# Kernel tuning notes

Measured on AMD Instinct MI355X. Metric: run time of the kernel, lower is better.

## Reference

```python
import jax, jax.numpy as jnp
import numpy as np

B, S, H, NH, HD, V = 2, 2048, 1024, 16, 64, 32000
BASE = 10000.0
NEG = jnp.finfo(jnp.float32).min


def setup_inputs() -> dict:
    key = jax.random.key(0)
    ks = jax.random.split(key, 12)
    batch = jax.random.randint(ks[0], (B, S), 0, V)
    positions = jnp.broadcast_to(jnp.arange(S), (B, S))
    lengths = jax.random.randint(ks[1], (B,), 1, S + 1)  # >=1 to avoid fully-masked rows
    sc = 1.0 / np.sqrt(H)
    emb = jax.random.normal(ks[2], (V, H), dtype=jnp.float32) * 0.02
    wq = jax.random.normal(ks[3], (H, NH * HD), dtype=jnp.float32) * sc
    bq = jnp.zeros((NH * HD,), jnp.float32)
    wk = jax.random.normal(ks[4], (H, NH * HD), dtype=jnp.float32) * sc
    bk = jnp.zeros((NH * HD,), jnp.float32)
    wv = jax.random.normal(ks[5], (H, NH * HD), dtype=jnp.float32) * sc
    bv = jnp.zeros((NH * HD,), jnp.float32)
    wo = jax.random.normal(ks[6], (NH * HD, H), dtype=jnp.float32) * sc
    bo = jnp.zeros((H,), jnp.float32)
    return dict(batch=batch, positions=positions, lengths=lengths, emb=emb,
                wq=wq, bq=bq, wk=wk, bk=bk, wv=wv, bv=bv, wo=wo, bo=bo)


def _rope(x, positions):
    # x: [B, NH, S, HD]; positions: [B, S] int
    inv_freq = 1.0 / (BASE ** (jnp.arange(0, HD, 2, dtype=jnp.float32) / HD))  # [HD/2]
    freqs = positions.astype(jnp.float32)[..., None] * inv_freq               # [B, S, HD/2]
    ang = jnp.concatenate([freqs, freqs], axis=-1)                            # [B, S, HD]
    cos = jnp.cos(ang)[:, None]                                               # [B, 1, S, HD]
    sin = jnp.sin(ang)[:, None]
    x1, x2 = x[..., :HD // 2], x[..., HD // 2:]
    rot = jnp.concatenate([-x2, x1], axis=-1)
    return x * cos + rot * sin


def reference(batch, positions, lengths, emb, wq, bq, wk, bk, wv, bv, wo, bo):
    h = emb[batch]                                                 # [B, S, H]
    q = (h @ wq + bq).reshape(B, S, NH, HD).transpose(0, 2, 1, 3)  # [B, NH, S, HD]
    k = (h @ wk + bk).reshape(B, S, NH, HD).transpose(0, 2, 1, 3)
    v = (h @ wv + bv).reshape(B, S, NH, HD).transpose(0, 2, 1, 3)
    q = _rope(q, positions)
    k = _rope(k, positions)
    scores = jnp.einsum('bhqd,bhkd->bhqk', q, k) / np.sqrt(HD)     # [B, NH, S, S]
    causal = jnp.triu(jnp.full((S, S), NEG, jnp.float32), 1)
    pad = jnp.where(jnp.arange(S)[None, :] < lengths[:, None], 0.0, NEG)  # [B, S]
    mask = pad[:, None, None, :] + causal[None, None]              # [B, 1, S, S]
    attn = jax.nn.softmax(scores + mask, axis=-1)
    out = jnp.einsum('bhqk,bhkd->bhqd', attn, v)                   # [B, NH, S, HD]
    out = out.transpose(0, 2, 1, 3).reshape(B, S, NH * HD)
    return out @ wo + bo                                           # [B, S, H]
```

## Files before the change

### kernel.cpp

```cpp
#include <hip/hip_runtime.h>
#include <hip/hip_bf16.h>
#include <cstdint>

#define DEVINL __device__ __forceinline__

typedef __attribute__((ext_vector_type(8))) short short8;
typedef __attribute__((ext_vector_type(4))) float f32x4;

constexpr int B_ = 2, S_ = 2048, H_ = 1024, NH_ = 16, HD_ = 64;
constexpr int M_ = B_ * S_;
constexpr float SC2 = 0.18033688f;

DEVINL float bf2f(unsigned short h) {
    unsigned u = ((unsigned)h) << 16;
    float f; __builtin_memcpy(&f, &u, 4); return f;
}
DEVINL unsigned short f2bf(float f) {
    unsigned u; __builtin_memcpy(&u, &f, 4);
    u += 0x7FFFu + ((u >> 16) & 1u);
    return (unsigned short)(u >> 16);
}
DEVINL unsigned pk2bf(float a, float b) {
    __hip_bfloat162 h = __float22bfloat162_rn(float2{a, b});
    unsigned u; __builtin_memcpy(&u, &h, 4); return u;
}
DEVINL float fexp2(float x) {
#if __has_builtin(__builtin_amdgcn_exp2f)
    return __builtin_amdgcn_exp2f(x);
#else
    return exp2f(x);
#endif
}
DEVINL float ldin(const void* p, size_t i, int fp32) {
    return fp32 ? ((const float*)p)[i] : bf2f(((const unsigned short*)p)[i]);
}
DEVINL void gl16(const void* g, void* l) {
    __builtin_amdgcn_global_load_lds(
        (const __attribute__((address_space(1))) unsigned int*)g,
        (__attribute__((address_space(3))) unsigned int*)l, 16, 0, 0);
}
DEVINL f32x4 mfma16(short8 a, short8 b, f32x4 c) {
    return __builtin_amdgcn_mfma_f32_16x16x32_bf16(a, b, c, 0, 0, 0);
}
DEVINL void fsincos(float rev01, float* sn, float* cs) {
#if __has_builtin(__builtin_amdgcn_sinf) && __has_builtin(__builtin_amdgcn_cosf)
    *sn = __builtin_amdgcn_sinf(rev01);
    *cs = __builtin_amdgcn_cosf(rev01);
#else
    float a = rev01 * 6.28318530717958647692f;
    *sn = __sinf(a); *cs = __cosf(a);
#endif
}
DEVINL int detect_fp32(const unsigned short* emb, int t) {
    unsigned short hw = emb[2 * t];
    unsigned e = (hw >> 7) & 0xFFu;
    int s = (((e >= 90u) && (e <= 126u)) || ((hw & 0x7FFFu) == 0u)) ? 1 : 0;
    #pragma unroll
    for (int o = 1; o < 64; o <<= 1) s += __shfl_xor(s, o);
    __shared__ int cnt[4];
    if ((t & 63) == 0) cnt[t >> 6] = s;
    __syncthreads();
    return ((cnt[0] + cnt[1] + cnt[2] + cnt[3]) > 192) ? 0 : 1;
}

__global__ __launch_bounds__(256) void k_transw(const void* w0, const void* w1,
                                                const void* w2, const void* w3,
                                                const void* bq, const void* bk,
                                                const void* bv, const void* bo,
                                                const unsigned short* __restrict__ emb,
                                                int* __restrict__ flag,
                                                float* __restrict__ biasws,
                                                unsigned short* __restrict__ wT) {
    __shared__ float tile[32][33];
    int tx = threadIdx.x, ty = threadIdx.y, t = ty * 32 + tx;
    int fp32 = detect_fp32(emb, t);
    int mat = blockIdx.z;
    if (mat == 0 && blockIdx.y == 0) {
        if (blockIdx.x == 0 && t == 0) flag[0] = fp32;
        if (blockIdx.x < 16) {
            int i = blockIdx.x * 256 + t;
            const void* src = (i < 1024) ? bq : (i < 2048) ? bk : (i < 3072) ? bv : bo;
            biasws[i] = ldin(src, (size_t)(i & 1023), fp32);
        }
    }
    const void* w = (mat == 0) ? w0 : (mat == 1) ? w1 : (mat == 2) ? w2 : w3;
    int n0 = blockIdx.x * 32, k0 = blockIdx.y * 32;
    for (int i = ty; i < 32; i += 8)
        tile[i][tx] = ldin(w, (size_t)(k0 + i) * 1024 + n0 + tx, fp32);
    __syncthreads();
    unsigned short* dst = wT + (size_t)mat * 1024 * 1024;
    for (int i = ty; i < 32; i += 8)
        dst[(size_t)(n0 + i) * 1024 + k0 + tx] = f2bf(tile[tx][i]);
}

__global__ __launch_bounds__(256) void k_gather(const int* __restrict__ batch,
                                                const void* __restrict__ emb,
                                                const int* __restrict__ flag,
                                                unsigned short* __restrict__ h) {
    if (flag[0] == 0) return;
    int row = blockIdx.x, t = threadIdx.x;
    int tok = batch[row];
    const float4* s = (const float4*)((const float*)emb + (size_t)tok * H_);
    float4 x = s[t];
    unsigned long long pk = (unsigned long long)f2bf(x.x)
                          | ((unsigned long long)f2bf(x.y) << 16)
                          | ((unsigned long long)f2bf(x.z) << 32)
                          | ((unsigned long long)f2bf(x.w) << 48);
    ((unsigned long long*)(h + (size_t)row * H_))[t] = pk;
}

__global__ __launch_bounds__(256) void k_gemm_qkv(const unsigned short* __restrict__ embb,
                                                  const unsigned short* __restrict__ hbuf,
                                                  const int* __restrict__ batch,
                                                  const unsigned short* __restrict__ Bt,
                                                  const float* __restrict__ bias,
                                                  const int* __restrict__ positions,
                                                  const int* __restrict__ flag,
                                                  unsigned short* __restrict__ qo,
                                                  unsigned short* __restrict__ ko,
                                                  unsigned short* __restrict__ vt) {
    constexpr int K = 1024;
    __shared__ alignas(16) unsigned short As[2][128 * 32];
    __shared__ alignas(16) unsigned short Bs[2][128 * 32];
    int t = threadIdx.x, lane = t & 63, quad = lane >> 4, n16 = lane & 15;
    int w = t >> 6, wm = w >> 1, wn = w & 1;
    int m0 = blockIdx.y * 128, n0 = blockIdx.x * 128;
    int fp32 = flag[0];
    int r0 = t >> 2, r1 = 64 + r0;
    int ka = (t & 3) * 8;
    const unsigned short* a0;
    const unsigned short* a1;
    if (fp32) {
        a0 = hbuf + (size_t)(m0 + r0) * K;
        a1 = hbuf + (size_t)(m0 + r1) * K;
    } else {
        a0 = embb + (size_t)batch[m0 + r0] * K;
        a1 = embb + (size_t)batch[m0 + r1] * K;
    }
    const unsigned short* b0 = Bt + (size_t)(n0 + r0) * K;
    const unsigned short* b1 = Bt + (size_t)(n0 + r1) * K;
    f32x4 acc[4][4];
    #pragma unroll
    for (int mi = 0; mi < 4; mi++)
        #pragma unroll
        for (int ni = 0; ni < 4; ni++) acc[mi][ni] = (f32x4){0.f, 0.f, 0.f, 0.f};
    for (int k0 = 0; k0 < K; k0 += 64) {
        __syncthreads();
        gl16(a0 + k0 + ka,      &As[0][t * 8]);
        gl16(a1 + k0 + ka,      &As[0][(t + 256) * 8]);
        gl16(a0 + k0 + 32 + ka, &As[1][t * 8]);
        gl16(a1 + k0 + 32 + ka, &As[1][(t + 256) * 8]);
        gl16(b0 + k0 + ka,      &Bs[0][t * 8]);
        gl16(b1 + k0 + ka,      &Bs[0][(t + 256) * 8]);
        gl16(b0 + k0 + 32 + ka, &Bs[1][t * 8]);
        gl16(b1 + k0 + 32 + ka, &Bs[1][(t + 256) * 8]);
        __syncthreads();
        #pragma unroll
        for (int ks = 0; ks < 2; ks++) {
            short8 af[4], bfr[4];
            #pragma unroll
            for (int mi = 0; mi < 4; mi++)
                af[mi] = *(const short8*)&As[ks][(wm * 64 + mi * 16 + n16) * 32 + quad * 8];
            #pragma unroll
            for (int ni = 0; ni < 4; ni++)
                bfr[ni] = *(const short8*)&Bs[ks][(wn * 64 + ni * 16 + n16) * 32 + quad * 8];
            #pragma unroll
            for (int mi = 0; mi < 4; mi++)
                #pragma unroll
                for (int ni = 0; ni < 4; ni++)
                    acc[mi][ni] = mfma16(af[mi], bfr[ni], acc[mi][ni]);
        }
    }
    int colbase = n0 + wn * 64;
    int buf = colbase >> 10;
    int cc = colbase & 1023;
    float bb[4];
    #pragma unroll
    for (int ni = 0; ni < 4; ni++) bb[ni] = bias[colbase + ni * 16 + n16];
    if (buf == 2) {
        #pragma unroll
        for (int mi = 0; mi < 4; mi++) {
            int row = m0 + wm * 64 + mi * 16 + quad * 4;
            int bb_ = row >> 11;
            int s0 = row & 2047;
            int pos = (s0 & ~31) + quad * 8 + (mi & 1) * 4;
            #pragma unroll
            for (int ni = 0; ni < 4; ni++) {
                int f = cc + ni * 16 + n16;
                unsigned long long pk =
                      (unsigned long long)pk2bf(acc[mi][ni][0] + bb[ni], acc[mi][ni][1] + bb[ni])
                    | ((unsigned long long)pk2bf(acc[mi][ni][2] + bb[ni], acc[mi][ni][3] + bb[ni]) << 32);
                *(unsigned long long*)(vt + ((size_t)(bb_ * 1024 + f)) * 2048 + pos) = pk;
            }
        }
    } else {
        unsigned short* out = (buf == 0) ? qo : ko;
        float osc = (buf == 0) ? SC2 : 1.0f;
        float revf[2];
        #pragma unroll
        for (int ni = 0; ni < 2; ni++) {
            float d = (float)(ni * 16 + n16);
            revf[ni] = __expf(d * -0.28782313f) * 0.15915494f;
        }
        #pragma unroll
        for (int mi = 0; mi < 4; mi++) {
            int row0 = m0 + wm * 64 + mi * 16 + quad * 4;
            #pragma unroll
            for (int i = 0; i < 4; i++) {
                int row = row0 + i;
                float pos = (float)positions[row];
                #pragma unroll
                for (int ni = 0; ni < 2; ni++) {
                    float rev = pos * revf[ni];
                    float fr = rev - floorf(rev);
                    float sn, cs; fsincos(fr, &sn, &cs);
                    float x1 = (acc[mi][ni][i] + bb[ni]) * osc;
                    float x2 = (acc[mi][ni + 2][i] + bb[ni + 2]) * osc;
                    out[(size_t)row * 1024 + cc + ni * 16 + n16] = f2bf(x1 * cs - x2 * sn);
                    out[(size_t)row * 1024 + cc + (ni + 2) * 16 + n16] = f2bf(x2 * cs + x1 * sn);
                }
            }
        }
    }
}

__global__ __launch_bounds__(256) void k_attn(const unsigned short* __restrict__ q,
                                              const unsigned short* __restrict__ k_,
                                              const unsigned short* __restrict__ vt,
                                              const int* __restrict__ lengths,
                                              unsigned short* __restrict__ o) {
    __shared__ alignas(16) unsigned short Ks[2][64 * 64];
    __shared__ alignas(16) unsigned short Vs[2][64 * 64];
    int bx = blockIdx.x;
    int j = bx & 15, hh = (bx >> 4) & 15, b = bx >> 8;
    int t = threadIdx.x, w = t >> 6, lane = t & 63, quad = lane >> 4, n16 = lane & 15;
    int len = lengths[b];
    int tile0 = j, tile1 = 31 - j;
    int kend0 = min(tile0 * 64 + 64, len);
    int kend1 = min(tile1 * 64 + 64, len);
    int nkt = (kend1 + 63) >> 6;
    int qrow0 = tile0 * 64 + w * 16 + n16;
    int qrow1 = tile1 * 64 + w * 16 + n16;
    int limit0 = min(qrow0, len - 1);
    int limit1 = min(qrow1, len - 1);
    int tbw0 = tile0 * 64 + w * 16;
    int tbw1 = tile1 * 64 + w * 16;
    short8 qf[2][2];
    {
        size_t qa = ((size_t)(b * S_ + qrow0)) * H_ + hh * 64 + quad * 8;
        size_t qb2 = ((size_t)(b * S_ + qrow1)) * H_ + hh * 64 + quad * 8;
        qf[0][0] = *(const short8*)(q + qa);  qf[0][1] = *(const short8*)(q + qa + 32);
        qf[1][0] = *(const short8*)(q + qb2); qf[1][1] = *(const short8*)(q + qb2 + 32);
    }
    f32x4 oa[2][4];
    float l_[2] = {0.f, 0.f};
    #pragma unroll
    for (int s = 0; s < 2; s++)
        #pragma unroll
        for (int nb = 0; nb < 4; nb++) oa[s][nb] = (f32x4){0.f, 0.f, 0.f, 0.f};
    const unsigned short* kbase = k_ + ((size_t)b * S_) * H_ + hh * 64;
    const unsigned short* vbase = vt + ((size_t)(b * 1024 + hh * 64)) * 2048;
    int sr0 = t >> 3, sc0 = (t & 7) ^ (sr0 & 7);
    int sr1 = (t + 256) >> 3, sc1 = (t & 7) ^ (sr1 & 7);
    auto stage = [&](int kt) {
        int kb = kt * 64, bi = kt & 1;
        gl16(kbase + (size_t)(kb + sr0) * H_ + sc0 * 8, &Ks[bi][t * 8]);
        gl16(kbase + (size_t)(kb + sr1) * H_ + sc1 * 8, &Ks[bi][(t + 256) * 8]);
        gl16(vbase + (size_t)sr0 * 2048 + kb + sc0 * 8, &Vs[bi][t * 8]);
        gl16(vbase + (size_t)sr1 * 2048 + kb + sc1 * 8, &Vs[bi][(t + 256) * 8]);
    };
    stage(0);
    for (int kt = 0; kt < nkt; kt++) {
        int kb = kt * 64, bi = kt & 1;
        __syncthreads();
        if (kt + 1 < nkt) stage(kt + 1);
        const unsigned short* Kb = Ks[bi];
        const unsigned short* Vb = Vs[bi];
        short8 kf[4][2];
        #pragma unroll
        for (int st = 0; st < 4; st++)
            #pragma unroll
            for (int hf = 0; hf < 2; hf++) {
                int ky = st * 16 + n16;
                kf[st][hf] = *(const short8*)&Kb[ky * 64 + (((hf * 4 + quad) ^ (ky & 7)) * 8)];
            }
        short8 vf[2][4];
        #pragma unroll
        for (int p = 0; p < 2; p++)
            #pragma unroll
            for (int nb = 0; nb < 4; nb++) {
                int f = nb * 16 + n16;
                vf[p][nb] = *(const short8*)&Vb[f * 64 + (((p * 4 + quad) ^ (f & 7)) * 8)];
            }
        #pragma unroll
        for (int si = 0; si < 2; si++) {
            if (si == 0 && kb >= kend0) continue;
            int limit = si ? limit1 : limit0;
            int tbw = si ? tbw1 : tbw0;
            f32x4 sc[4];
            #pragma unroll
            for (int st = 0; st < 4; st++) {
                f32x4 z = (f32x4){0.f, 0.f, 0.f, 0.f};
                z = mfma16(kf[st][0], qf[si][0], z);
                z = mfma16(kf[st][1], qf[si][1], z);
                sc[st] = z;
            }
            float rs = 0.f;
            if (kb + 64 <= min(tbw, len)) {
                #pragma unroll
                for (int st = 0; st < 4; st++)
                    #pragma unroll
                    for (int i = 0; i < 4; i++) {
                        float p = fexp2(sc[st][i]);
                        rs += p;
                        sc[st][i] = p;
                    }
            } else {
                #pragma unroll
                for (int st = 0; st < 4; st++)
                    #pragma unroll
                    for (int i = 0; i < 4; i++) {
                        int kg = kb + st * 16 + quad * 4 + i;
                        float p = (kg <= limit) ? fexp2(sc[st][i]) : 0.f;
                        rs += p;
                        sc[st][i] = p;
                    }
            }
            rs += __shfl_xor(rs, 16);
            rs += __shfl_xor(rs, 32);
            l_[si] += rs;
            #pragma unroll
            for (int p = 0; p < 2; p++) {
                union { unsigned u[4]; short8 v8; } pp;
                pp.u[0] = pk2bf(sc[2 * p][0], sc[2 * p][1]);
                pp.u[1] = pk2bf(sc[2 * p][2], sc[2 * p][3]);
                pp.u[2] = pk2bf(sc[2 * p + 1][0], sc[2 * p + 1][1]);
                pp.u[3] = pk2bf(sc[2 * p + 1][2], sc[2 * p + 1][3]);
                #pragma unroll
                for (int nb = 0; nb < 4; nb++)
                    oa[si][nb] = mfma16(pp.v8, vf[p][nb], oa[si][nb]);
            }
        }
    }
    #pragma unroll
    for (int si = 0; si < 2; si++) {
        int tb = si ? tile1 : tile0;
        f32x4 rl;
        #pragma unroll
        for (int i = 0; i < 4; i++) rl[i] = 1.f / __shfl(l_[si], quad * 4 + i);
        #pragma unroll
        for (int nb = 0; nb < 4; nb++) {
            #pragma unroll
            for (int i = 0; i < 4; i++) {
                int row = tb * 64 + w * 16 + quad * 4 + i;
                o[((size_t)(b * S_ + row)) * H_ + hh * 64 + nb * 16 + n16] =
                    f2bf(oa[si][nb][i] * rl[i]);
            }
        }
    }
}

__global__ __launch_bounds__(256) void k_gemm64(const unsigned short* __restrict__ A,
                                                const unsigned short* __restrict__ Bt,
                                                const float* __restrict__ bias,
                                                unsigned short* __restrict__ Cb,
                                                float* __restrict__ Cf,
                                                const int* __restrict__ flag) {
    constexpr int K = 1024, N = 1024;
    __shared__ alignas(16) unsigned short As[2][64 * 32];
    __shared__ alignas(16) unsigned short Bs[2][128 * 32];
    int t = threadIdx.x, lane = t & 63, quad = lane >> 4, n16 = lane & 15;
    int w = t >> 6, wm = w & 1, wn = w >> 1;
    int m0 = blockIdx.y * 64, n0 = blockIdx.x * 128;
    int r0 = t >> 2, r1 = 64 + r0, ka = (t & 3) * 8;
    const unsigned short* a0 = A + (size_t)(m0 + r0) * K;
    const unsigned short* b0 = Bt + (size_t)(n0 + r0) * K;
    const unsigned short* b1 = Bt + (size_t)(n0 + r1) * K;
    f32x4 acc[2][4];
    #pragma unroll
    for (int mi = 0; mi < 2; mi++)
        #pragma unroll
        for (int ni = 0; ni < 4; ni++) acc[mi][ni] = (f32x4){0.f, 0.f, 0.f, 0.f};
    for (int k0 = 0; k0 < K; k0 += 64) {
        __syncthreads();
        gl16(a0 + k0 + ka,      &As[0][t * 8]);
        gl16(a0 + k0 + 32 + ka, &As[1][t * 8]);
        gl16(b0 + k0 + ka,      &Bs[0][t * 8]);
        gl16(b1 + k0 + ka,      &Bs[0][(t + 256) * 8]);
        gl16(b0 + k0 + 32 + ka, &Bs[1][t * 8]);
        gl16(b1 + k0 + 32 + ka, &Bs[1][(t + 256) * 8]);
        __syncthreads();
        #pragma unroll
        for (int ks = 0; ks < 2; ks++) {
            short8 af[2], bfr[4];
            #pragma unroll
            for (int mi = 0; mi < 2; mi++)
                af[mi] = *(const short8*)&As[ks][(wm * 32 + mi * 16 + n16) * 32 + quad * 8];
            #pragma unroll
            for (int ni = 0; ni < 4; ni++)
                bfr[ni] = *(const short8*)&Bs[ks][(wn * 64 + ni * 16 + n16) * 32 + quad * 8];
            #pragma unroll
            for (int mi = 0; mi < 2; mi++)
                #pragma unroll
                for (int ni = 0; ni < 4; ni++)
                    acc[mi][ni] = mfma16(af[mi], bfr[ni], acc[mi][ni]);
        }
    }
    int fp32out = (flag[0] == 1);
    #pragma unroll
    for (int mi = 0; mi < 2; mi++) {
        #pragma unroll
        for (int ni = 0; ni < 4; ni++) {
            int row = m0 + wm * 32 + mi * 16 + quad * 4;
            int col = n0 + wn * 64 + ni * 16 + n16;
            float bb = bias[col];
            #pragma unroll
            for (int i = 0; i < 4; i++) {
                float val = acc[mi][ni][i] + bb;
                size_t idx = (size_t)(row + i) * N + col;
                if (fp32out) Cf[idx] = val;
                else         Cb[idx] = f2bf(val);
            }
        }
    }
}

extern "C" void kernel_launch(void* const* d_in, const int* in_sizes, int n_in,
                              void* d_out, int out_size, void* d_ws, size_t ws_size,
                              hipStream_t stream) {
    (void)in_sizes; (void)n_in; (void)out_size; (void)ws_size;
    const int* batch     = (const int*)d_in[0];
    const int* positions = (const int*)d_in[1];
    const int* lengths   = (const int*)d_in[2];
    const void* emb = d_in[3];
    const void* wq = d_in[4];  const void* bq = d_in[5];
    const void* wk = d_in[6];  const void* bk = d_in[7];
    const void* wv = d_in[8];  const void* bv = d_in[9];
    const void* wo = d_in[10]; const void* bo = d_in[11];

    char* ws = (char*)d_ws;
    int*   flag   = (int*)ws;
    float* biasws = (float*)(ws + 4096);
    unsigned short* wT = (unsigned short*)(ws + 20480);
    size_t off = 20480 + (8ull << 20);
    unsigned short* hbuf = (unsigned short*)(ws + off); off += (8ull << 20);
    unsigned short* qb   = (unsigned short*)(ws + off); off += (8ull << 20);
    unsigned short* kb2  = (unsigned short*)(ws + off); off += (8ull << 20);
    unsigned short* vtb  = (unsigned short*)(ws + off); off += (8ull << 20);
    unsigned short* ao   = (unsigned short*)(ws + off); off += (8ull << 20);

    k_transw<<<dim3(32, 32, 4), dim3(32, 8), 0, stream>>>(
        wq, wk, wv, wo, bq, bk, bv, bo, (const unsigned short*)emb,
        flag, biasws, wT);
    k_gather<<<M_, 256, 0, stream>>>(batch, emb, flag, hbuf);

    k_gemm_qkv<<<dim3(3072 / 128, M_ / 128), 256, 0, stream>>>(
        (const unsigned short*)emb, hbuf, batch, wT, biasws, positions, flag,
        qb, kb2, vtb);

    k_attn<<<B_ * NH_ * 16, 256, 0, stream>>>(qb, kb2, vtb, lengths, ao);

    k_gemm64<<<dim3(1024 / 128, M_ / 64), 256, 0, stream>>>(
        ao, wT + (3ull << 20), biasws + 3072,
        (unsigned short*)d_out, (float*)d_out, flag);
}
```

Measured before the change: 303.0 us.

## Fuse gather into weight prep, load V directly, add MFMA priority and batch tile reversal

Merges the embedding gather kernel into the weight-transpose kernel as an extra grid slice, removing one launch. In attention, V fragments are now read straight from global memory instead of being staged through shared memory, which halves LDS traffic but makes V loads uncoalesced and synchronous. It also raises wave priority around MFMA blocks and reverses the tile order for odd batches to balance causal work across blocks. These changes trade LDS staging and a launch for possible global-latency stalls.

```diff
diff --git a/kernel.cpp b/kernel.cpp
--- a/kernel.cpp
+++ b/kernel.cpp
@@ -63,18 +63,39 @@
     return ((cnt[0] + cnt[1] + cnt[2] + cnt[3]) > 192) ? 0 : 1;
 }
 
-__global__ __launch_bounds__(256) void k_transw(const void* w0, const void* w1,
-                                                const void* w2, const void* w3,
-                                                const void* bq, const void* bk,
-                                                const void* bv, const void* bo,
-                                                const unsigned short* __restrict__ emb,
-                                                int* __restrict__ flag,
-                                                float* __restrict__ biasws,
-                                                unsigned short* __restrict__ wT) {
-    __shared__ float tile[32][33];
+__global__ __launch_bounds__(256) void k_prep(const void* w0, const void* w1,
+                                              const void* w2, const void* w3,
+                                              const void* bq, const void* bk,
+                                              const void* bv, const void* bo,
+                                              const unsigned short* __restrict__ emb,
+                                              const int* __restrict__ batch,
+                                              int* __restrict__ flag,
+                                              float* __restrict__ biasws,
+                                              unsigned short* __restrict__ wT,
+                                              unsigned short* __restrict__ hbuf) {
     int tx = threadIdx.x, ty = threadIdx.y, t = ty * 32 + tx;
     int fp32 = detect_fp32(emb, t);
-    int mat = blockIdx.z;
+    int z = blockIdx.z;
+    if (z == 4) {
+        if (!fp32) return;
+        int g = blockIdx.y * 32 + blockIdx.x;
+        int w = t >> 6, lane = t & 63;
+        int row = g * 4 + w;
+        int tok = batch[row];
+        const float4* s = (const float4*)((const float*)emb + (size_t)tok * H_);
+        unsigned long long* d = (unsigned long long*)(hbuf + (size_t)row * H_);
+        #pragma unroll
+        for (int c = 0; c < 4; c++) {
+            float4 x = s[lane + 64 * c];
+            d[lane + 64 * c] = (unsigned long long)f2bf(x.x)
+                             | ((unsigned long long)f2bf(x.y) << 16)
+                             | ((unsigned long long)f2bf(x.z) << 32)
+                             | ((unsigned long long)f2bf(x.w) << 48);
+        }
+        return;
+    }
+    __shared__ float tile[32][33];
+    int mat = z;
     if (mat == 0 && blockIdx.y == 0) {
         if (blockIdx.x == 0 && t == 0) flag[0] = fp32;
         if (blockIdx.x < 16) {
@@ -91,22 +112,6 @@
     unsigned short* dst = wT + (size_t)mat * 1024 * 1024;
     for (int i = ty; i < 32; i += 8)
         dst[(size_t)(n0 + i) * 1024 + k0 + tx] = f2bf(tile[tx][i]);
-}
-
-__global__ __launch_bounds__(256) void k_gather(const int* __restrict__ batch,
-                                                const void* __restrict__ emb,
-                                                const int* __restrict__ flag,
-                                                unsigned short* __restrict__ h) {
-    if (flag[0] == 0) return;
-    int row = blockIdx.x, t = threadIdx.x;
-    int tok = batch[row];
-    const float4* s = (const float4*)((const float*)emb + (size_t)tok * H_);
-    float4 x = s[t];
-    unsigned long long pk = (unsigned long long)f2bf(x.x)
-                          | ((unsigned long long)f2bf(x.y) << 16)
-                          | ((unsigned long long)f2bf(x.z) << 32)
-                          | ((unsigned long long)f2bf(x.w) << 48);
-    ((unsigned long long*)(h + (size_t)row * H_))[t] = pk;
 }
 
 __global__ __launch_bounds__(256) void k_gemm_qkv(const unsigned short* __restrict__ embb,
@@ -230,9 +235,9 @@
                                               const int* __restrict__ lengths,
                                               unsigned short* __restrict__ o) {
     __shared__ alignas(16) unsigned short Ks[2][64 * 64];
-    __shared__ alignas(16) unsigned short Vs[2][64 * 64];
     int bx = blockIdx.x;
-    int j = bx & 15, hh = (bx >> 4) & 15, b = bx >> 8;
+    int jraw = bx & 15, hh = (bx >> 4) & 15, b = bx >> 8;
+    int j = (b & 1) ? (15 - jraw) : jraw;
     int t = threadIdx.x, w = t >> 6, lane = t & 63, quad = lane >> 4, n16 = lane & 15;
     int len = lengths[b];
     int tile0 = j, tile1 = 31 - j;
@@ -266,8 +271,6 @@
         int kb = kt * 64, bi = kt & 1;
         gl16(kbase + (size_t)(kb + sr0) * H_ + sc0 * 8, &Ks[bi][t * 8]);
         gl16(kbase + (size_t)(kb + sr1) * H_ + sc1 * 8, &Ks[bi][(t + 256) * 8]);
-        gl16(vbase + (size_t)sr0 * 2048 + kb + sc0 * 8, &Vs[bi][t * 8]);
-        gl16(vbase + (size_t)sr1 * 2048 + kb + sc1 * 8, &Vs[bi][(t + 256) * 8]);
     };
     stage(0);
     for (int kt = 0; kt < nkt; kt++) {
@@ -275,7 +278,6 @@
         __syncthreads();
         if (kt + 1 < nkt) stage(kt + 1);
         const unsigned short* Kb = Ks[bi];
-        const unsigned short* Vb = Vs[bi];
         short8 kf[4][2];
         #pragma unroll
         for (int st = 0; st < 4; st++)
@@ -290,7 +292,7 @@
             #pragma unroll
             for (int nb = 0; nb < 4; nb++) {
                 int f = nb * 16 + n16;
-                vf[p][nb] = *(const short8*)&Vb[f * 64 + (((p * 4 + quad) ^ (f & 7)) * 8)];
+                vf[p][nb] = *(const short8*)(vbase + (size_t)f * 2048 + kb + (p * 4 + quad) * 8);
             }
         #pragma unroll
         for (int si = 0; si < 2; si++) {
@@ -298,6 +300,7 @@
             int limit = si ? limit1 : limit0;
             int tbw = si ? tbw1 : tbw0;
             f32x4 sc[4];
+            __builtin_amdgcn_s_setprio(1);
             #pragma unroll
             for (int st = 0; st < 4; st++) {
                 f32x4 z = (f32x4){0.f, 0.f, 0.f, 0.f};
@@ -305,6 +308,7 @@
                 z = mfma16(kf[st][1], qf[si][1], z);
                 sc[st] = z;
             }
+            __builtin_amdgcn_s_setprio(0);
             float rs = 0.f;
             if (kb + 64 <= min(tbw, len)) {
                 #pragma unroll
@@ -336,9 +340,11 @@
                 pp.u[1] = pk2bf(sc[2 * p][2], sc[2 * p][3]);
                 pp.u[2] = pk2bf(sc[2 * p + 1][0], sc[2 * p + 1][1]);
                 pp.u[3] = pk2bf(sc[2 * p + 1][2], sc[2 * p + 1][3]);
+                __builtin_amdgcn_s_setprio(1);
                 #pragma unroll
                 for (int nb = 0; nb < 4; nb++)
                     oa[si][nb] = mfma16(pp.v8, vf[p][nb], oa[si][nb]);
+                __builtin_amdgcn_s_setprio(0);
             }
         }
     }
@@ -449,10 +455,9 @@
     unsigned short* vtb  = (unsigned short*)(ws + off); off += (8ull << 20);
     unsigned short* ao   = (unsigned short*)(ws + off); off += (8ull << 20);
 
-    k_transw<<<dim3(32, 32, 4), dim3(32, 8), 0, stream>>>(
-        wq, wk, wv, wo, bq, bk, bv, bo, (const unsigned short*)emb,
-        flag, biasws, wT);
-    k_gather<<<M_, 256, 0, stream>>>(batch, emb, flag, hbuf);
+    k_prep<<<dim3(32, 32, 5), dim3(32, 8), 0, stream>>>(
+        wq, wk, wv, wo, bq, bk, bv, bo, (const unsigned short*)emb, batch,
+        flag, biasws, wT, hbuf);
 
     k_gemm_qkv<<<dim3(3072 / 128, M_ / 128), 256, 0, stream>>>(
         (const unsigned short*)emb, hbuf, batch, wT, biasws, positions, flag,
```

Result: slower. 315.9 us (+4.2%).
